# Kernel optimization log

Measured on AMD Instinct MI355X. Metric: run time of the kernel, lower is better.

The kernel has to match this reference:

```python
import jax, jax.numpy as jnp
import numpy as np
from jax import lax

BLUR_SIGMA = 21
OUT_SIZE = 256
PAD = 30
BLUR_SIZE = int(np.floor(BLUR_SIGMA * 3))  # 63 -> 127-tap filter


def _gauss_filter():
    x = jnp.arange(-BLUR_SIZE, BLUR_SIZE + 1, dtype=jnp.float32)
    f = jnp.exp2(-jnp.square(x / BLUR_SIGMA))
    return f / jnp.sum(f)


def _resize_axis(x, out_size, axis):
    # torch bilinear (align_corners=False, no antialias) along one axis
    in_size = x.shape[axis]
    scale = in_size / out_size
    coords = (jnp.arange(out_size, dtype=jnp.float32) + 0.5) * scale - 0.5
    coords = jnp.clip(coords, 0.0, in_size - 1)
    lo = jnp.floor(coords).astype(jnp.int32)
    hi = jnp.minimum(lo + 1, in_size - 1)
    w = coords - lo.astype(jnp.float32)
    bshape = [1] * x.ndim
    bshape[axis] = out_size
    w = w.reshape(bshape).astype(x.dtype)
    xlo = jnp.take(x, lo, axis=axis)
    xhi = jnp.take(x, hi, axis=axis)
    return xlo * (1 - w) + xhi * w


def _bilinear_resize(x, out_h, out_w):
    x = _resize_axis(x, out_h, axis=2)
    x = _resize_axis(x, out_w, axis=3)
    return x


def _sep_blur(x, f):
    # depthwise separable FIR, zero padding k//2 (same size), as upfirdn2d.filter2d
    C = x.shape[1]
    k = f.shape[0]
    dn = ('NCHW', 'OIHW', 'NCHW')
    kw = jnp.tile(f.reshape(1, 1, 1, k), (C, 1, 1, 1)).astype(x.dtype)
    x = lax.conv_general_dilated(x, kw, (1, 1), [(0, 0), (k // 2, k // 2)],
                                 feature_group_count=C, dimension_numbers=dn)
    kh = jnp.tile(f.reshape(1, 1, k, 1), (C, 1, 1, 1)).astype(x.dtype)
    x = lax.conv_general_dilated(x, kh, (1, 1), [(k // 2, k // 2), (0, 0)],
                                 feature_group_count=C, dimension_numbers=dn)
    return x


def setup_inputs() -> dict:
    key = jax.random.key(0)
    img = jax.random.normal(key, (16, 3, 1024, 1024), dtype=jnp.float32)
    return {"img_tensor": img}


def reference(img_tensor):
    x = _bilinear_resize(img_tensor, OUT_SIZE, OUT_SIZE)               # [B,3,256,256]
    x = jnp.pad(x, ((0, 0), (0, 0), (PAD, PAD), (PAD, PAD)), mode='reflect')  # [B,3,316,316]
    x = _sep_blur(x, _gauss_filter())                                  # [B,3,316,316]
    return x[:, :, PAD:-PAD, PAD:-PAD]                                 # [B,3,256,256]
```

## Files before the change

kernel.cpp:

```cpp
#include <hip/hip_runtime.h>
#include <stdint.h>


#define CHTOT 48
#define IN_W  1024
#define OUT_W 256
#define PADW  316
#define KTAP  127

typedef _Float16 half_t;
typedef __attribute__((ext_vector_type(4))) _Float16 half4;

__device__ __forceinline__ float4 f4fma(float4 v, float w, float4 a) {
    a.x = fmaf(v.x, w, a.x); a.y = fmaf(v.y, w, a.y);
    a.z = fmaf(v.z, w, a.z); a.w = fmaf(v.w, w, a.w);
    return a;
}

__device__ __forceinline__ void compute_weights(float* W, float* partial, int tid) {
    float e = 0.f;
    if (tid < KTAP) {
        float q = (float)(tid - 63) * (1.0f / 21.0f);
        e = exp2f(-q * q);
    }
    float s = e;
    #pragma unroll
    for (int off = 32; off >= 1; off >>= 1) s += __shfl_down(s, off, 64);
    if ((tid & 63) == 0) partial[tid >> 6] = s;
    if (tid < 136) W[tid] = 0.f;
    __syncthreads();
    float S = partial[0] + partial[1] + partial[2] + partial[3];
    if (tid < KTAP) W[3 + tid] = e / S;
    __syncthreads();
}

__global__ __launch_bounds__(256) void hblur_kernel(const float* __restrict__ in,
                                                    half_t* __restrict__ H) {
    __shared__ float4 W4[34];
    __shared__ float4 R4s[4][96];
    __shared__ float  partial[4];
    int tid = threadIdx.x;
    compute_weights((float*)W4, partial, tid);

    int ch = blockIdx.y;
    int p0 = blockIdx.x * 4;
    float* Rext = (float*)R4s;

    {
        int j = tid;
        const size_t chbase = (size_t)ch * (IN_W * IN_W);
        #pragma unroll
        for (int rr = 0; rr < 4; ++rr) {
            int pr = p0 + rr - 30;
            int r = pr < 0 ? -pr : (pr > 255 ? 510 - pr : pr);
            const float4* row1 = (const float4*)(in + chbase + (size_t)(4 * r + 1) * IN_W);
            const float4* row2 = row1 + (IN_W / 4);
            float4 a = row1[j];
            float4 b = row2[j];
            float m1 = 0.5f * a.y + 0.5f * b.y;
            float m2 = 0.5f * a.z + 0.5f * b.z;
            Rext[rr * 384 + 63 + j] = 0.5f * m1 + 0.5f * m2;
        }
    }
    __syncthreads();
    #pragma unroll
    for (int rr = 0; rr < 4; ++rr) {
        float* Rx = Rext + rr * 384;
        if (tid < 33) {
            Rx[tid] = 0.f;
        } else if (tid < 63) {
            Rx[tid] = Rx[126 - tid];
        } else if (tid >= 64 && tid < 94) {
            int q = 286 + (tid - 64);
            Rx[33 + q] = Rx[603 - q];
        } else if (tid >= 96 && tid < 131) {
            Rx[253 + tid] = 0.f;
        }
    }
    __syncthreads();

    int g = tid >> 6;
    int l = tid & 63;
    const float4* Rv = (const float4*)(Rext + g * 384);
    float acc0 = 0.f, acc1 = 0.f, acc2 = 0.f, acc3 = 0.f;
    float4 wlo = W4[0];
    #pragma unroll
    for (int i = 0; i < 33; ++i) {
        float4 whi = W4[i + 1];
        float4 v = Rv[l + i];
        acc0 = fmaf(v.x, wlo.w, acc0); acc0 = fmaf(v.y, whi.x, acc0);
        acc0 = fmaf(v.z, whi.y, acc0); acc0 = fmaf(v.w, whi.z, acc0);
        acc1 = fmaf(v.x, wlo.z, acc1); acc1 = fmaf(v.y, wlo.w, acc1);
        acc1 = fmaf(v.z, whi.x, acc1); acc1 = fmaf(v.w, whi.y, acc1);
        acc2 = fmaf(v.x, wlo.y, acc2); acc2 = fmaf(v.y, wlo.z, acc2);
        acc2 = fmaf(v.z, wlo.w, acc2); acc2 = fmaf(v.w, whi.x, acc2);
        acc3 = fmaf(v.x, wlo.x, acc3); acc3 = fmaf(v.y, wlo.y, acc3);
        acc3 = fmaf(v.z, wlo.z, acc3); acc3 = fmaf(v.w, wlo.w, acc3);
        wlo = whi;
    }
    int p = p0 + g;
    half4 hv;
    hv.x = (half_t)acc0; hv.y = (half_t)acc1; hv.z = (half_t)acc2; hv.w = (half_t)acc3;
    ((half4*)H)[((size_t)ch * PADW + p) * 64 + l] = hv;
}

__global__ __launch_bounds__(256) void vblur_kernel(const half_t* __restrict__ H,
                                                    float* __restrict__ out) {
    __shared__ float4 W4[34];
    __shared__ float  partial[4];
    __shared__ float4 T[192 * 16];
    int tid = threadIdx.x;
    compute_weights((float*)W4, partial, tid);

    int ch = blockIdx.y;
    int xt = blockIdx.x & 3;
    int yt = blockIdx.x >> 2;
    int x0h4 = xt * 16;
    int y0 = yt * 64;

    const half4* H4 = (const half4*)H;
    for (int idx = tid; idx < 192 * 16; idx += 256) {
        int rr = idx >> 4, fx = idx & 15;
        int r = y0 - 33 + rr;
        float4 v = make_float4(0.f, 0.f, 0.f, 0.f);
        if (r >= 0 && r < PADW) {
            half4 h = H4[((size_t)ch * PADW + r) * 64 + x0h4 + fx];
            v = make_float4((float)h.x, (float)h.y, (float)h.z, (float)h.w);
        }
        T[idx] = v;
    }
    __syncthreads();

    int cg = tid & 15;
    int g  = tid >> 4;
    float4 acc0 = make_float4(0,0,0,0), acc1 = acc0, acc2 = acc0, acc3 = acc0;
    float4 wlo = W4[0];
    #pragma unroll
    for (int i = 0; i < 33; ++i) {
        float4 whi = W4[i + 1];
        int base = (4 * g + 4 * i) * 16 + cg;
        float4 v0 = T[base];
        float4 v1 = T[base + 16];
        float4 v2 = T[base + 32];
        float4 v3 = T[base + 48];
        acc0 = f4fma(v0, wlo.w, acc0); acc0 = f4fma(v1, whi.x, acc0);
        acc0 = f4fma(v2, whi.y, acc0); acc0 = f4fma(v3, whi.z, acc0);
        acc1 = f4fma(v0, wlo.z, acc1); acc1 = f4fma(v1, wlo.w, acc1);
        acc1 = f4fma(v2, whi.x, acc1); acc1 = f4fma(v3, whi.y, acc1);
        acc2 = f4fma(v0, wlo.y, acc2); acc2 = f4fma(v1, wlo.z, acc2);
        acc2 = f4fma(v2, wlo.w, acc2); acc2 = f4fma(v3, whi.x, acc2);
        acc3 = f4fma(v0, wlo.x, acc3); acc3 = f4fma(v1, wlo.y, acc3);
        acc3 = f4fma(v2, wlo.z, acc3); acc3 = f4fma(v3, wlo.w, acc3);
        wlo = whi;
    }

    float4* o4 = (float4*)out;
    float4 accs[4] = {acc0, acc1, acc2, acc3};
    #pragma unroll
    for (int j = 0; j < 4; ++j) {
        int y = y0 + 4 * g + j;
        o4[((size_t)ch * OUT_W + y) * 64 + xt * 16 + cg] = accs[j];
    }
}

extern "C" void kernel_launch(void* const* d_in, const int* in_sizes, int n_in,
                              void* d_out, int out_size, void* d_ws, size_t ws_size,
                              hipStream_t stream) {
    const float* in = (const float*)d_in[0];
    float* out = (float*)d_out;
    half_t* H = (half_t*)d_ws;

    hblur_kernel<<<dim3(79, CHTOT), dim3(256), 0, stream>>>(in, H);
    vblur_kernel<<<dim3(16, CHTOT), dim3(256), 0, stream>>>(H, out);
}
```

Measured before the change: 272.2 us.

## Fuse horizontal and vertical blur into one kernel with shared-memory intermediate

Merges the separate horizontal-blur and vertical-blur kernels into a single kernel. Each block owns a 64-column strip of one channel across all 316 padded rows, keeping the half-precision intermediate in LDS instead of a global workspace. This removes the global round trip for the intermediate and one launch. In exchange the grid shrinks to 4x48 blocks, far fewer than the number of CUs, and each block recomputes its horizontal halo and re-gathers the input samples that neighbouring strips also read. The horizontal input staging is also stored as fp16, adding extra rounding.

```diff
diff --git a/kernel.cpp b/kernel.cpp
--- a/kernel.cpp
+++ b/kernel.cpp
@@ -16,150 +16,133 @@
     a.z = fmaf(v.z, w, a.z); a.w = fmaf(v.w, w, a.w);
     return a;
 }
-
-__device__ __forceinline__ void compute_weights(float* W, float* partial, int tid) {
-    float e = 0.f;
-    if (tid < KTAP) {
-        float q = (float)(tid - 63) * (1.0f / 21.0f);
-        e = exp2f(-q * q);
-    }
-    float s = e;
-    #pragma unroll
-    for (int off = 32; off >= 1; off >>= 1) s += __shfl_down(s, off, 64);
-    if ((tid & 63) == 0) partial[tid >> 6] = s;
-    if (tid < 136) W[tid] = 0.f;
-    __syncthreads();
-    float S = partial[0] + partial[1] + partial[2] + partial[3];
-    if (tid < KTAP) W[3 + tid] = e / S;
-    __syncthreads();
+__device__ __forceinline__ float4 h2f4(half4 h) {
+    return make_float4((float)h.x, (float)h.y, (float)h.z, (float)h.w);
 }
 
-__global__ __launch_bounds__(256) void hblur_kernel(const float* __restrict__ in,
-                                                    half_t* __restrict__ H) {
+__global__ __launch_bounds__(512) void fused_kernel(const float* __restrict__ in,
+                                                    float* __restrict__ out) {
     __shared__ float4 W4[34];
-    __shared__ float4 R4s[4][96];
-    __shared__ float  partial[4];
-    int tid = threadIdx.x;
-    compute_weights((float*)W4, partial, tid);
+    __shared__ float  partial[8];
+    __shared__ half_t Rext[8][4][192];
+    __shared__ half_t Hs[384 * 68];
 
-    int ch = blockIdx.y;
-    int p0 = blockIdx.x * 4;
-    float* Rext = (float*)R4s;
+    const int tid  = threadIdx.x;
+    const int w    = tid >> 6;
+    const int lane = tid & 63;
+    float* W = (float*)W4;
 
     {
-        int j = tid;
-        const size_t chbase = (size_t)ch * (IN_W * IN_W);
+        float e = 0.f;
+        if (tid < KTAP) {
+            float q = (float)(tid - 63) * (1.0f / 21.0f);
+            e = exp2f(-q * q);
+        }
+        float s = e;
         #pragma unroll
-        for (int rr = 0; rr < 4; ++rr) {
-            int pr = p0 + rr - 30;
-            int r = pr < 0 ? -pr : (pr > 255 ? 510 - pr : pr);
-            const float4* row1 = (const float4*)(in + chbase + (size_t)(4 * r + 1) * IN_W);
-            const float4* row2 = row1 + (IN_W / 4);
-            float4 a = row1[j];
-            float4 b = row2[j];
-            float m1 = 0.5f * a.y + 0.5f * b.y;
-            float m2 = 0.5f * a.z + 0.5f * b.z;
-            Rext[rr * 384 + 63 + j] = 0.5f * m1 + 0.5f * m2;
+        for (int off = 32; off >= 1; off >>= 1) s += __shfl_down(s, off, 64);
+        if (lane == 0) partial[w] = s;
+        if (tid < 34) W4[tid] = make_float4(0.f, 0.f, 0.f, 0.f);
+        for (int i = tid; i < 384 * 68 / 2; i += 512) ((unsigned int*)Hs)[i] = 0u;
+        __syncthreads();
+        float S = 0.f;
+        #pragma unroll
+        for (int k = 0; k < 8; ++k) S += partial[k];
+        if (tid < KTAP) W[3 + tid] = e / S;
+        __syncthreads();
+    }
+
+    const int X0 = blockIdx.x * 64;
+    const size_t chbase = (size_t)blockIdx.y * (IN_W * IN_W);
+    const float4* in4 = (const float4*)(in + chbase);
+
+    for (int it = 0; it < 10; ++it) {
+        int quad = it * 8 + w;
+        bool active = quad < 79;
+        if (active) {
+            int p_base = quad * 4;
+            #pragma unroll
+            for (int k = 0; k < 12; ++k) {
+                int s = k * 64 + lane;
+                int rr = s / 192;
+                int c  = s - rr * 192;
+                int q  = X0 - 33 + c;
+                float val = 0.f;
+                if (q >= 0 && q < PADW) {
+                    int yq = q - 30;
+                    int xr = yq < 0 ? -yq : (yq > 255 ? 510 - yq : yq);
+                    int pp = p_base + rr - 30;
+                    int r  = pp < 0 ? -pp : (pp > 255 ? 510 - pp : pp);
+                    float4 a = in4[(4 * r + 1) * (IN_W / 4) + xr];
+                    float4 b = in4[(4 * r + 2) * (IN_W / 4) + xr];
+                    float m1 = 0.5f * a.y + 0.5f * b.y;
+                    float m2 = 0.5f * a.z + 0.5f * b.z;
+                    val = 0.5f * m1 + 0.5f * m2;
+                }
+                Rext[w][rr][c] = (half_t)val;
+            }
         }
-    }
-    __syncthreads();
-    #pragma unroll
-    for (int rr = 0; rr < 4; ++rr) {
-        float* Rx = Rext + rr * 384;
-        if (tid < 33) {
-            Rx[tid] = 0.f;
-        } else if (tid < 63) {
-            Rx[tid] = Rx[126 - tid];
-        } else if (tid >= 64 && tid < 94) {
-            int q = 286 + (tid - 64);
-            Rx[33 + q] = Rx[603 - q];
-        } else if (tid >= 96 && tid < 131) {
-            Rx[253 + tid] = 0.f;
+        __syncthreads();
+        if (active) {
+            int rr = lane >> 4, u = lane & 15;
+            const half4* Rv = (const half4*)(&Rext[w][rr][0]);
+            float acc0 = 0.f, acc1 = 0.f, acc2 = 0.f, acc3 = 0.f;
+            float4 wlo = W4[0];
+            #pragma unroll
+            for (int i = 0; i < 33; ++i) {
+                float4 whi = W4[i + 1];
+                half4 h = Rv[u + i];
+                float vx = (float)h.x, vy = (float)h.y, vz = (float)h.z, vw = (float)h.w;
+                acc0 = fmaf(vx, wlo.w, acc0); acc0 = fmaf(vy, whi.x, acc0);
+                acc0 = fmaf(vz, whi.y, acc0); acc0 = fmaf(vw, whi.z, acc0);
+                acc1 = fmaf(vx, wlo.z, acc1); acc1 = fmaf(vy, wlo.w, acc1);
+                acc1 = fmaf(vz, whi.x, acc1); acc1 = fmaf(vw, whi.y, acc1);
+                acc2 = fmaf(vx, wlo.y, acc2); acc2 = fmaf(vy, wlo.z, acc2);
+                acc2 = fmaf(vz, wlo.w, acc2); acc2 = fmaf(vw, whi.x, acc2);
+                acc3 = fmaf(vx, wlo.x, acc3); acc3 = fmaf(vy, wlo.y, acc3);
+                acc3 = fmaf(vz, wlo.z, acc3); acc3 = fmaf(vw, wlo.w, acc3);
+                wlo = whi;
+            }
+            int p = quad * 4 + rr;
+            half4 hv;
+            hv.x = (half_t)acc0; hv.y = (half_t)acc1;
+            hv.z = (half_t)acc2; hv.w = (half_t)acc3;
+            *(half4*)(&Hs[(33 + p) * 68 + 4 * u]) = hv;
         }
     }
     __syncthreads();
 
-    int g = tid >> 6;
-    int l = tid & 63;
-    const float4* Rv = (const float4*)(Rext + g * 384);
-    float acc0 = 0.f, acc1 = 0.f, acc2 = 0.f, acc3 = 0.f;
-    float4 wlo = W4[0];
+    const int cg = tid & 15;
+    float4* out4 = (float4*)out;
     #pragma unroll
-    for (int i = 0; i < 33; ++i) {
-        float4 whi = W4[i + 1];
-        float4 v = Rv[l + i];
-        acc0 = fmaf(v.x, wlo.w, acc0); acc0 = fmaf(v.y, whi.x, acc0);
-        acc0 = fmaf(v.z, whi.y, acc0); acc0 = fmaf(v.w, whi.z, acc0);
-        acc1 = fmaf(v.x, wlo.z, acc1); acc1 = fmaf(v.y, wlo.w, acc1);
-        acc1 = fmaf(v.z, whi.x, acc1); acc1 = fmaf(v.w, whi.y, acc1);
-        acc2 = fmaf(v.x, wlo.y, acc2); acc2 = fmaf(v.y, wlo.z, acc2);
-        acc2 = fmaf(v.z, wlo.w, acc2); acc2 = fmaf(v.w, whi.x, acc2);
-        acc3 = fmaf(v.x, wlo.x, acc3); acc3 = fmaf(v.y, wlo.y, acc3);
-        acc3 = fmaf(v.z, wlo.z, acc3); acc3 = fmaf(v.w, wlo.w, acc3);
-        wlo = whi;
-    }
-    int p = p0 + g;
-    half4 hv;
-    hv.x = (half_t)acc0; hv.y = (half_t)acc1; hv.z = (half_t)acc2; hv.w = (half_t)acc3;
-    ((half4*)H)[((size_t)ch * PADW + p) * 64 + l] = hv;
-}
-
-__global__ __launch_bounds__(256) void vblur_kernel(const half_t* __restrict__ H,
-                                                    float* __restrict__ out) {
-    __shared__ float4 W4[34];
-    __shared__ float  partial[4];
-    __shared__ float4 T[192 * 16];
-    int tid = threadIdx.x;
-    compute_weights((float*)W4, partial, tid);
-
-    int ch = blockIdx.y;
-    int xt = blockIdx.x & 3;
-    int yt = blockIdx.x >> 2;
-    int x0h4 = xt * 16;
-    int y0 = yt * 64;
-
-    const half4* H4 = (const half4*)H;
-    for (int idx = tid; idx < 192 * 16; idx += 256) {
-        int rr = idx >> 4, fx = idx & 15;
-        int r = y0 - 33 + rr;
-        float4 v = make_float4(0.f, 0.f, 0.f, 0.f);
-        if (r >= 0 && r < PADW) {
-            half4 h = H4[((size_t)ch * PADW + r) * 64 + x0h4 + fx];
-            v = make_float4((float)h.x, (float)h.y, (float)h.z, (float)h.w);
+    for (int ph = 0; ph < 2; ++ph) {
+        int gl = ph * 32 + (tid >> 4);
+        float4 acc0 = make_float4(0,0,0,0), acc1 = acc0, acc2 = acc0, acc3 = acc0;
+        float4 wlo = W4[0];
+        #pragma unroll
+        for (int i = 0; i < 33; ++i) {
+            float4 whi = W4[i + 1];
+            int base = (4 * gl + 4 * i) * 68 + 4 * cg;
+            float4 v0 = h2f4(*(const half4*)(&Hs[base]));
+            float4 v1 = h2f4(*(const half4*)(&Hs[base + 68]));
+            float4 v2 = h2f4(*(const half4*)(&Hs[base + 136]));
+            float4 v3 = h2f4(*(const half4*)(&Hs[base + 204]));
+            acc0 = f4fma(v0, wlo.w, acc0); acc0 = f4fma(v1, whi.x, acc0);
+            acc0 = f4fma(v2, whi.y, acc0); acc0 = f4fma(v3, whi.z, acc0);
+            acc1 = f4fma(v0, wlo.z, acc1); acc1 = f4fma(v1, wlo.w, acc1);
+            acc1 = f4fma(v2, whi.x, acc1); acc1 = f4fma(v3, whi.y, acc1);
+            acc2 = f4fma(v0, wlo.y, acc2); acc2 = f4fma(v1, wlo.z, acc2);
+            acc2 = f4fma(v2, wlo.w, acc2); acc2 = f4fma(v3, whi.x, acc2);
+            acc3 = f4fma(v0, wlo.x, acc3); acc3 = f4fma(v1, wlo.y, acc3);
+            acc3 = f4fma(v2, wlo.z, acc3); acc3 = f4fma(v3, wlo.w, acc3);
+            wlo = whi;
         }
-        T[idx] = v;
-    }
-    __syncthreads();
-
-    int cg = tid & 15;
-    int g  = tid >> 4;
-    float4 acc0 = make_float4(0,0,0,0), acc1 = acc0, acc2 = acc0, acc3 = acc0;
-    float4 wlo = W4[0];
-    #pragma unroll
-    for (int i = 0; i < 33; ++i) {
-        float4 whi = W4[i + 1];
-        int base = (4 * g + 4 * i) * 16 + cg;
-        float4 v0 = T[base];
-        float4 v1 = T[base + 16];
-        float4 v2 = T[base + 32];
-        float4 v3 = T[base + 48];
-        acc0 = f4fma(v0, wlo.w, acc0); acc0 = f4fma(v1, whi.x, acc0);
-        acc0 = f4fma(v2, whi.y, acc0); acc0 = f4fma(v3, whi.z, acc0);
-        acc1 = f4fma(v0, wlo.z, acc1); acc1 = f4fma(v1, wlo.w, acc1);
-        acc1 = f4fma(v2, whi.x, acc1); acc1 = f4fma(v3, whi.y, acc1);
-        acc2 = f4fma(v0, wlo.y, acc2); acc2 = f4fma(v1, wlo.z, acc2);
-        acc2 = f4fma(v2, wlo.w, acc2); acc2 = f4fma(v3, whi.x, acc2);
-        acc3 = f4fma(v0, wlo.x, acc3); acc3 = f4fma(v1, wlo.y, acc3);
-        acc3 = f4fma(v2, wlo.z, acc3); acc3 = f4fma(v3, wlo.w, acc3);
-        wlo = whi;
-    }
-
-    float4* o4 = (float4*)out;
-    float4 accs[4] = {acc0, acc1, acc2, acc3};
-    #pragma unroll
-    for (int j = 0; j < 4; ++j) {
-        int y = y0 + 4 * g + j;
-        o4[((size_t)ch * OUT_W + y) * 64 + xt * 16 + cg] = accs[j];
+        float4 accs[4] = {acc0, acc1, acc2, acc3};
+        #pragma unroll
+        for (int j = 0; j < 4; ++j) {
+            int y = 4 * gl + j;
+            out4[((size_t)blockIdx.y * OUT_W + y) * 64 + blockIdx.x * 16 + cg] = accs[j];
+        }
     }
 }
 
@@ -168,8 +151,5 @@
                               hipStream_t stream) {
     const float* in = (const float*)d_in[0];
     float* out = (float*)d_out;
-    half_t* H = (half_t*)d_ws;
-
-    hblur_kernel<<<dim3(79, CHTOT), dim3(256), 0, stream>>>(in, H);
-    vblur_kernel<<<dim3(16, CHTOT), dim3(256), 0, stream>>>(H, out);
+    fused_kernel<<<dim3(4, CHTOT), dim3(512), 0, stream>>>(in, out);
 }
```

New measurement: 345.7 us. +27.0%, slower.
